# Performance work log

Measured on AMD Instinct MI355X. Metric: run time of the kernel, lower is better.

Reference implementation:

```python
import jax, jax.numpy as jnp
import numpy as np

B_, L_, D_MODEL = 2, 1024, 1024
D_STATE, EXPAND = 16, 2
D_INNER = EXPAND * D_MODEL            # 2048
DT_RANK = (D_MODEL + 15) // 16        # 64


def setup_inputs() -> dict:
    key = jax.random.key(0)
    ks = jax.random.split(key, 6)
    dt_min, dt_max, dt_floor = 1e-3, 0.1, 1e-4
    dt = jnp.exp(jax.random.uniform(ks[4], (D_INNER,)) * (np.log(dt_max) - np.log(dt_min)) + np.log(dt_min))
    dt = jnp.clip(dt, dt_floor)
    inv_dt = dt + jnp.log(-jnp.expm1(-dt))  # softplus^{-1}(dt), matches torch init
    A_log = jnp.log(jnp.broadcast_to(jnp.arange(1, D_STATE + 1, dtype=jnp.float32), (D_INNER, D_STATE)))
    s_in = 1.0 / np.sqrt(D_MODEL)
    s_inner = 1.0 / np.sqrt(D_INNER)
    return {
        "input_states": jax.random.normal(ks[0], (B_, L_, D_MODEL), jnp.float32),
        "in_proj_w": jax.random.normal(ks[1], (2 * D_INNER, D_MODEL), jnp.float32) * s_in,
        "x_proj_w": jax.random.normal(ks[2], (DT_RANK + 2 * D_STATE, D_INNER), jnp.float32) * s_inner,
        "dt_proj_w": jax.random.uniform(ks[3], (D_INNER, DT_RANK), jnp.float32, -1.0, 1.0) * (DT_RANK ** -0.5),
        "dt_proj_b": inv_dt.astype(jnp.float32),
        "A_log": A_log,
        "D": jnp.ones((D_INNER,), jnp.float32),
        "out_proj_w": jax.random.normal(ks[5], (D_MODEL, D_INNER), jnp.float32) * s_inner,
        "context_len": 2,
    }


def _linear_scan(a, u, axis):
    # h_t = a_t * h_{t-1} + u_t, h_{-1} = 0, parallel associative scan
    def comb(left, right):
        a_l, b_l = left
        a_r, b_r = right
        return (a_r * a_l, a_r * b_l + b_r)
    return jax.lax.associative_scan(comb, (a, u), axis=axis)[1]


def reference(input_states, in_proj_w, x_proj_w, dt_proj_w, dt_proj_b, A_log, D, out_proj_w, context_len):
    # context_len <= 2 => both tree refines use the chain tree; feature_out = 1.3 * chain_tree_scan
    assert context_len <= 2, "MST branch (context_len>2) not modeled"
    b, L, _ = input_states.shape
    proj = input_states @ in_proj_w.T                       # (b, L, 2*d_inner)
    hidden, gate = jnp.split(proj, 2, axis=-1)              # (b, L, d)
    hs = jnp.swapaxes(hidden, 1, 2)                         # (b, d, L)
    ssm = hidden @ x_proj_w.T                               # (b, L, dt_rank+2n)
    dt, Bm, Cm = jnp.split(ssm, [DT_RANK, DT_RANK + D_STATE], axis=-1)
    dt = jax.nn.softplus(dt @ dt_proj_w.T + dt_proj_b)      # (b, L, d)
    dt_bdl = jnp.swapaxes(dt, 1, 2)                         # (b, d, L)
    A = -jnp.exp(A_log)                                     # (d, n)
    discrete_A = jnp.exp(A[None, :, None, :] * dt_bdl[:, :, :, None])           # (b, d, L, n)
    deltaB_u = dt_bdl[:, :, :, None] * Bm[:, None, :, :] * hs[:, :, :, None]    # (b, d, L, n)
    # chain tree filter: out[t] = sum_s prod(path A) * u[s] = fwd_scan + bwd_scan - u
    fwd = _linear_scan(discrete_A, deltaB_u, axis=2)
    a_rev = jnp.roll(jnp.flip(discrete_A, axis=2), 1, axis=2)  # == `weight` in source
    bwd = jnp.flip(_linear_scan(a_rev, jnp.flip(deltaB_u, axis=2), axis=2), axis=2)
    feature_out = (fwd + bwd - deltaB_u) * 1.3               # feature_out1 + 0.3*feature_out2
    y = jnp.einsum("bdln,bln->bdl", feature_out, Cm)         # (b, d, L)
    scan_output = (y + hs * D[None, :, None]) * jax.nn.silu(jnp.swapaxes(gate, 1, 2))
    return jnp.swapaxes(scan_output, 1, 2) @ out_proj_w.T    # (b, L, d_model)
```

## Files before the change

kernel.cpp:

```cpp
#include <hip/hip_runtime.h>
#include <hip/hip_bf16.h>
#include <cstdint>
#include <cstddef>

typedef __hip_bfloat16 bf16;
typedef __attribute__((ext_vector_type(8))) short short8v;
typedef __attribute__((ext_vector_type(4))) float f32x4;

__global__ __launch_bounds__(256)
void cast_bf16(const float* __restrict__ in, ushort* __restrict__ out, int n4)
{
    const int i = blockIdx.x * 256 + threadIdx.x;
    if (i >= n4) return;
    const float4 v = ((const float4*)in)[i];
    ushort4 o;
    bf16 h;
    h = __float2bfloat16(v.x); o.x = *(ushort*)&h;
    h = __float2bfloat16(v.y); o.y = *(ushort*)&h;
    h = __float2bfloat16(v.z); o.z = *(ushort*)&h;
    h = __float2bfloat16(v.w); o.w = *(ushort*)&h;
    ((ushort4*)out)[i] = o;
}

__global__ __launch_bounds__(256)
void gemm_bf16_mfma(const bf16* __restrict__ A, int lda,
                    const bf16* __restrict__ W, int ldw,
                    float* __restrict__ C, int ldc, int K)
{
    __shared__ short Asl[128 * 32];
    __shared__ short Wsl[128 * 32];
    const int tid = threadIdx.x;
    const int lane = tid & 63, wave = tid >> 6;
    const int row0 = blockIdx.y * 128, col0 = blockIdx.x * 128;
    const int wr = wave >> 1, wc = wave & 1;
    const int lr = lane & 15, lq = lane >> 4;

    f32x4 acc[4][4] = {};

    for (int k0 = 0; k0 < K; k0 += 32) {
#pragma unroll
        for (int i = 0; i < 2; ++i) {
            const int o = ((i * 4 + wave) << 9) + lane * 8;
            const int r = o >> 5, kk = o & 31;
            __builtin_amdgcn_global_load_lds(
                (const __attribute__((address_space(1))) void*)(A + (size_t)(row0 + r) * lda + k0 + kk),
                (__attribute__((address_space(3))) void*)(Asl + (((i * 4 + wave) << 9))),
                16, 0, 0);
            __builtin_amdgcn_global_load_lds(
                (const __attribute__((address_space(1))) void*)(W + (size_t)(col0 + r) * ldw + k0 + kk),
                (__attribute__((address_space(3))) void*)(Wsl + (((i * 4 + wave) << 9))),
                16, 0, 0);
        }
        __syncthreads();

        short8v af[4], wf[4];
#pragma unroll
        for (int m = 0; m < 4; ++m)
            af[m] = *(const short8v*)&Asl[(wr * 64 + m * 16 + lr) * 32 + lq * 8];
#pragma unroll
        for (int n = 0; n < 4; ++n)
            wf[n] = *(const short8v*)&Wsl[(wc * 64 + n * 16 + lr) * 32 + lq * 8];
#pragma unroll
        for (int m = 0; m < 4; ++m)
#pragma unroll
            for (int n = 0; n < 4; ++n)
                acc[m][n] = __builtin_amdgcn_mfma_f32_16x16x32_bf16(af[m], wf[n], acc[m][n], 0, 0, 0);
        __syncthreads();
    }

#pragma unroll
    for (int m = 0; m < 4; ++m) {
        const int r = row0 + wr * 64 + m * 16 + lq * 4;
#pragma unroll
        for (int n = 0; n < 4; ++n) {
            const int c = col0 + wc * 64 + n * 16 + lr;
#pragma unroll
            for (int j = 0; j < 4; ++j)
                C[(size_t)(r + j) * ldc + c] = acc[m][n][j];
        }
    }
}

#define BM 64
#define BN 64
#define BK 16
#define BMP 68
#define BNP 68

__global__ __launch_bounds__(256)
void gemm_nt(const float* __restrict__ A, int lda,
             const float* __restrict__ W, int ldw,
             float* __restrict__ C, int ldc,
             int M, int N, int K,
             const float* __restrict__ bias, int mode)
{
    __shared__ float As[BK][BMP];
    __shared__ float Ws[BK][BNP];

    const int tid  = threadIdx.x;
    const int row0 = blockIdx.y * BM;
    const int col0 = blockIdx.x * BN;
    const int lr = tid >> 2;
    const int lk = (tid & 3) << 2;
    const int tx = tid & 15;
    const int ty = tid >> 4;

    float acc[4][4];
#pragma unroll
    for (int i = 0; i < 4; ++i)
#pragma unroll
        for (int j = 0; j < 4; ++j) acc[i][j] = 0.f;

    for (int k0 = 0; k0 < K; k0 += BK) {
        float4 av = make_float4(0.f, 0.f, 0.f, 0.f);
        float4 wv = make_float4(0.f, 0.f, 0.f, 0.f);
        const int ar = row0 + lr;
        if (ar < M) av = *(const float4*)(A + (size_t)ar * lda + k0 + lk);
        const int wr = col0 + lr;
        if (wr < N) wv = *(const float4*)(W + (size_t)wr * ldw + k0 + lk);

        As[lk + 0][lr] = av.x; As[lk + 1][lr] = av.y;
        As[lk + 2][lr] = av.z; As[lk + 3][lr] = av.w;
        Ws[lk + 0][lr] = wv.x; Ws[lk + 1][lr] = wv.y;
        Ws[lk + 2][lr] = wv.z; Ws[lk + 3][lr] = wv.w;
        __syncthreads();

#pragma unroll
        for (int kk = 0; kk < BK; ++kk) {
            float4 a = *(const float4*)&As[kk][ty * 4];
            float4 w = *(const float4*)&Ws[kk][tx * 4];
            float ai[4] = {a.x, a.y, a.z, a.w};
            float wj[4] = {w.x, w.y, w.z, w.w};
#pragma unroll
            for (int i = 0; i < 4; ++i)
#pragma unroll
                for (int j = 0; j < 4; ++j)
                    acc[i][j] = fmaf(ai[i], wj[j], acc[i][j]);
        }
        __syncthreads();
    }

#pragma unroll
    for (int i = 0; i < 4; ++i) {
        const int r = row0 + ty * 4 + i;
        if (r >= M) continue;
#pragma unroll
        for (int j = 0; j < 4; ++j) {
            const int c = col0 + tx * 4 + j;
            if (c >= N) continue;
            float v = acc[i][j];
            if (mode == 1) {
                v += bias[c];
                v = (v > 20.f) ? v : log1pf(__expf(v));
            }
            C[(size_t)r * ldc + c] = v;
        }
    }
}

__global__ __launch_bounds__(256)
void gemm_nt_splitk(const float* __restrict__ A, int lda,
                    const float* __restrict__ W, int ldw,
                    float* __restrict__ P,
                    int M, int N, int K, int ksplit)
{
    __shared__ float As[BK][BMP];
    __shared__ float Ws[BK][BNP];

    const int tid  = threadIdx.x;
    const int row0 = blockIdx.y * BM;
    const int col0 = blockIdx.x * BN;
    const int z    = blockIdx.z;
    const int k0s = z * ksplit, k0e = k0s + ksplit;
    const int lr = tid >> 2;
    const int lk = (tid & 3) << 2;
    const int tx = tid & 15;
    const int ty = tid >> 4;

    float acc[4][4];
#pragma unroll
    for (int i = 0; i < 4; ++i)
#pragma unroll
        for (int j = 0; j < 4; ++j) acc[i][j] = 0.f;

    for (int k0 = k0s; k0 < k0e; k0 += BK) {
        float4 av = make_float4(0.f, 0.f, 0.f, 0.f);
        float4 wv = make_float4(0.f, 0.f, 0.f, 0.f);
        const int ar = row0 + lr;
        if (ar < M) av = *(const float4*)(A + (size_t)ar * lda + k0 + lk);
        const int wr = col0 + lr;
        if (wr < N) wv = *(const float4*)(W + (size_t)wr * ldw + k0 + lk);

        As[lk + 0][lr] = av.x; As[lk + 1][lr] = av.y;
        As[lk + 2][lr] = av.z; As[lk + 3][lr] = av.w;
        Ws[lk + 0][lr] = wv.x; Ws[lk + 1][lr] = wv.y;
        Ws[lk + 2][lr] = wv.z; Ws[lk + 3][lr] = wv.w;
        __syncthreads();

#pragma unroll
        for (int kk = 0; kk < BK; ++kk) {
            float4 a = *(const float4*)&As[kk][ty * 4];
            float4 w = *(const float4*)&Ws[kk][tx * 4];
            float ai[4] = {a.x, a.y, a.z, a.w};
            float wj[4] = {w.x, w.y, w.z, w.w};
#pragma unroll
            for (int i = 0; i < 4; ++i)
#pragma unroll
                for (int j = 0; j < 4; ++j)
                    acc[i][j] = fmaf(ai[i], wj[j], acc[i][j]);
        }
        __syncthreads();
    }

    float* C = P + (size_t)z * M * N;
#pragma unroll
    for (int i = 0; i < 4; ++i) {
        const int r = row0 + ty * 4 + i;
        if (r >= M) continue;
#pragma unroll
        for (int j = 0; j < 4; ++j) {
            const int c = col0 + tx * 4 + j;
            if (c >= N) continue;
            C[(size_t)r * N + c] = acc[i][j];
        }
    }
}

__global__ __launch_bounds__(256)
void reduce_splitk(const float* __restrict__ P, float* __restrict__ out,
                   int total, int nsplit)
{
    const int i = blockIdx.x * 256 + threadIdx.x;
    if (i >= total) return;
    float s = 0.f;
    for (int z = 0; z < nsplit; ++z) s += P[i + (size_t)z * total];
    out[i] = s;
}

#define NC 32
#define CL 32
#define DI 2048
#define NST 16

__global__ __launch_bounds__(256)
void scan_chunk_local(const float* __restrict__ proj,
                      const float* __restrict__ ssm,
                      const float* __restrict__ dtb,
                      const float* __restrict__ A_log,
                      float* __restrict__ Pf, float* __restrict__ He,
                      float* __restrict__ Pb, float* __restrict__ Gs,
                      float* __restrict__ dtbound)
{
    const int g = blockIdx.x * 256 + threadIdx.x;
    const int d = g & (DI - 1);
    const int r = g >> 11;
    const int c = r & (NC - 1);
    const int b = r >> 5;
    const int t0 = c * CL;
    const size_t rowbase = (size_t)b * 1024;

    float Av[NST];
#pragma unroll
    for (int n = 0; n < NST; ++n) Av[n] = -__expf(A_log[d * NST + n]);

    float h[NST], pf[NST];
#pragma unroll
    for (int n = 0; n < NST; ++n) { h[n] = 0.f; pf[n] = 1.f; }
    for (int t = t0; t < t0 + CL; ++t) {
        const size_t row = rowbase + t;
        const float dtv = dtb[row * DI + d];
        const float hv  = proj[row * 4096 + d];
        const float dh  = dtv * hv;
#pragma unroll
        for (int n = 0; n < NST; ++n) {
            const float Bv = ssm[row * 96 + 64 + n];
            const float dA = __expf(Av[n] * dtv);
            h[n] = fmaf(dA, h[n], dh * Bv);
            pf[n] *= dA;
        }
    }
    const size_t ibase = ((size_t)((b * NC + c) * NST) << 11) + d;
#pragma unroll
    for (int n = 0; n < NST; ++n) {
        Pf[ibase + ((size_t)n << 11)] = pf[n];
        He[ibase + ((size_t)n << 11)] = h[n];
    }

    float dtn = INFINITY;
    const int t1 = t0 + CL;
    if (t1 < 1024) dtn = dtb[(rowbase + t1) * DI + d];
    dtbound[(size_t)(b * NC + c) * DI + d] = dtn;

    float gq[NST], pb[NST], dan[NST];
#pragma unroll
    for (int n = 0; n < NST; ++n) {
        gq[n] = 0.f; pb[n] = 1.f;
        dan[n] = __expf(Av[n] * dtn);
    }
    for (int t = t0 + CL - 1; t >= t0; --t) {
        const size_t row = rowbase + t;
        const float dtv = dtb[row * DI + d];
        const float hv  = proj[row * 4096 + d];
        const float dh  = dtv * hv;
#pragma unroll
        for (int n = 0; n < NST; ++n) {
            const float Bv = ssm[row * 96 + 64 + n];
            gq[n] = fmaf(dan[n], gq[n], dh * Bv);
            pb[n] *= dan[n];
            dan[n] = __expf(Av[n] * dtv);
        }
    }
#pragma unroll
    for (int n = 0; n < NST; ++n) {
        Pb[ibase + ((size_t)n << 11)] = pb[n];
        Gs[ibase + ((size_t)n << 11)] = gq[n];
    }
}

__global__ __launch_bounds__(256)
void scan_combine(const float* __restrict__ Pf, float* __restrict__ He,
                  const float* __restrict__ Pb, float* __restrict__ Gs)
{
    const int g = blockIdx.x * 256 + threadIdx.x;
    const int d = g & (DI - 1);
    const int r = g >> 11;
    const int n = r & (NST - 1);
    const int b = r >> 4;
    const size_t base = ((size_t)(b * NC * NST + n) << 11) + d;
    const size_t cstride = (size_t)NST << 11;

    float H = 0.f;
    for (int c = 0; c < NC; ++c) {
        const size_t i = base + (size_t)c * cstride;
        const float p = Pf[i], e = He[i];
        He[i] = H;
        H = fmaf(p, H, e);
    }
    float G = 0.f;
    for (int c = NC - 1; c >= 0; --c) {
        const size_t i = base + (size_t)c * cstride;
        const float p = Pb[i], s = Gs[i];
        Gs[i] = G;
        G = fmaf(p, G, s);
    }
}

__global__ __launch_bounds__(256)
void scan_apply(const float* __restrict__ proj,
                const float* __restrict__ ssm,
                const float* __restrict__ dtb,
                const float* __restrict__ A_log,
                const float* __restrict__ Dvec,
                const float* __restrict__ He,
                const float* __restrict__ Gs,
                const float* __restrict__ dtbound,
                ushort* __restrict__ sob)
{
    __shared__ float ybuf[256][CL + 1];
    const int tid = threadIdx.x;
    const int g = blockIdx.x * 256 + tid;
    const int d = g & (DI - 1);
    const int r = g >> 11;
    const int c = r & (NC - 1);
    const int b = r >> 5;
    const int t0 = c * CL;
    const size_t rowbase = (size_t)b * 1024;

    float Av[NST];
#pragma unroll
    for (int n = 0; n < NST; ++n) Av[n] = -__expf(A_log[d * NST + n]);
    const size_t ibase = ((size_t)((b * NC + c) * NST) << 11) + d;

    float h[NST];
#pragma unroll
    for (int n = 0; n < NST; ++n) h[n] = He[ibase + ((size_t)n << 11)];
    for (int t = t0; t < t0 + CL; ++t) {
        const size_t row = rowbase + t;
        const float dtv = dtb[row * DI + d];
        const float hv  = proj[row * 4096 + d];
        const float dh  = dtv * hv;
        float y = 0.f;
#pragma unroll
        for (int n = 0; n < NST; ++n) {
            const float Bv = ssm[row * 96 + 64 + n];
            const float Cv = ssm[row * 96 + 80 + n];
            const float dA = __expf(Av[n] * dtv);
            h[n] = fmaf(dA, h[n], dh * Bv);
            y = fmaf(h[n], Cv, y);
        }
        ybuf[tid][t - t0] = y;
    }

    float gq[NST], dan[NST];
#pragma unroll
    for (int n = 0; n < NST; ++n) gq[n] = Gs[ibase + ((size_t)n << 11)];
    {
        const float dtn = dtbound[(size_t)(b * NC + c) * DI + d];
#pragma unroll
        for (int n = 0; n < NST; ++n) dan[n] = __expf(Av[n] * dtn);
    }
    const float Dd = Dvec[d];
    for (int t = t0 + CL - 1; t >= t0; --t) {
        const size_t row = rowbase + t;
        const float dtv = dtb[row * DI + d];
        const float hv  = proj[row * 4096 + d];
        const float dh  = dtv * hv;
        float acc = 0.f;
#pragma unroll
        for (int n = 0; n < NST; ++n) {
            const float Bv = ssm[row * 96 + 64 + n];
            const float Cv = ssm[row * 96 + 80 + n];
            const float u  = dh * Bv;
            gq[n] = fmaf(dan[n], gq[n], u);
            dan[n] = __expf(Av[n] * dtv);
            acc = fmaf(gq[n] - u, Cv, acc);
        }
        const float y   = (ybuf[tid][t - t0] + acc) * 1.3f;
        const float gv  = proj[row * 4096 + DI + d];
        const float sil = gv / (1.f + __expf(-gv));
        const float val = (y + hv * Dd) * sil;
        bf16 hb = __float2bfloat16(val);
        sob[row * DI + d] = *(ushort*)&hb;
    }
}

extern "C" void kernel_launch(void* const* d_in, const int* in_sizes, int n_in,
                              void* d_out, int out_size, void* d_ws, size_t ws_size,
                              hipStream_t stream)
{
    const float* x     = (const float*)d_in[0];
    const float* Win   = (const float*)d_in[1];
    const float* Wx    = (const float*)d_in[2];
    const float* Wdt   = (const float*)d_in[3];
    const float* bdt   = (const float*)d_in[4];
    const float* A_log = (const float*)d_in[5];
    const float* Dv    = (const float*)d_in[6];
    const float* Wout  = (const float*)d_in[7];
    float* out = (float*)d_out;

    const int B = 2, L = 1024, DM = 1024;
    const int M = B * L;

    float* proj = (float*)d_ws;
    float* ssm  = proj + (size_t)M * 2 * DI;
    float* dtb  = ssm  + (size_t)M * 96;
    float* Pf   = dtb  + (size_t)M * DI;
    float* He   = Pf   + (size_t)B * NC * NST * DI;
    float* Pb   = He   + (size_t)B * NC * NST * DI;
    float* Gs   = Pb   + (size_t)B * NC * NST * DI;
    float* dtbd = Gs   + (size_t)B * NC * NST * DI;
    ushort* xb    = (ushort*)(dtbd + (size_t)B * NC * DI);
    ushort* Winb  = xb    + (size_t)M * DM;
    ushort* Woutb = Winb  + (size_t)(2 * DI) * DM;
    ushort* sob   = Woutb + (size_t)DM * DI;
    float* part = Pf;

    dim3 blk(256);

    cast_bf16<<<dim3((M * DM / 4) / 256), blk, 0, stream>>>(x, xb, M * DM / 4);
    cast_bf16<<<dim3((2 * DI * DM / 4) / 256), blk, 0, stream>>>(Win, Winb, 2 * DI * DM / 4);
    cast_bf16<<<dim3((DM * DI / 4) / 256), blk, 0, stream>>>(Wout, Woutb, DM * DI / 4);

    gemm_bf16_mfma<<<dim3((2 * DI) / 128, M / 128), blk, 0, stream>>>(
        (const bf16*)xb, DM, (const bf16*)Winb, DM, proj, 2 * DI, DM);

    gemm_nt_splitk<<<dim3(2, M / BM, 16), blk, 0, stream>>>(
        proj, 2 * DI, Wx, DI, part, M, 96, DI, DI / 16);
    reduce_splitk<<<dim3((M * 96 + 255) / 256), blk, 0, stream>>>(
        part, ssm, M * 96, 16);

    gemm_nt<<<dim3(DI / BN, M / BM), blk, 0, stream>>>(
        ssm, 96, Wdt, 64, dtb, DI, M, DI, 64, bdt, 1);

    scan_chunk_local<<<dim3((B * DI * NC) / 256), blk, 0, stream>>>(
        proj, ssm, dtb, A_log, Pf, He, Pb, Gs, dtbd);
    scan_combine<<<dim3((B * DI * NST) / 256), blk, 0, stream>>>(Pf, He, Pb, Gs);
    scan_apply<<<dim3((B * DI * NC) / 256), blk, 0, stream>>>(
        proj, ssm, dtb, A_log, Dv, He, Gs, dtbd, sob);

    gemm_bf16_mfma<<<dim3(DM / 128, M / 128), blk, 0, stream>>>(
        (const bf16*)sob, DI, (const bf16*)Woutb, DI, out, DM, DI);
}
```

Before: 315.0 us.

## Split scan state dimension across thread pairs and fuse backward chunk pass

Each (batch, chunk, channel) scan task is now handled by two adjacent threads, each owning 8 of the 16 state entries, with y and acc partial sums combined via lane shuffles. This doubles the thread count and halves per-thread registers and serial work to raise occupancy. The chunk-local kernel also drops its separate backward pass, computing the backward chunk sum and product algebraically inside the forward loop with a running prefix product. Adjacent lanes now read the same d, so dtb/proj loads are duplicated and less coalesced per thread, and only half the lanes write the output.

```diff
diff --git a/kernel.cpp b/kernel.cpp
--- a/kernel.cpp
+++ b/kernel.cpp
@@ -252,68 +252,64 @@
                       float* __restrict__ dtbound)
 {
     const int g = blockIdx.x * 256 + threadIdx.x;
-    const int d = g & (DI - 1);
-    const int r = g >> 11;
+    const int half = g & 1;
+    const int d = (g >> 1) & (DI - 1);
+    const int r = g >> 12;
     const int c = r & (NC - 1);
     const int b = r >> 5;
     const int t0 = c * CL;
+    const int n0 = half * 8;
     const size_t rowbase = (size_t)b * 1024;
 
-    float Av[NST];
-#pragma unroll
-    for (int n = 0; n < NST; ++n) Av[n] = -__expf(A_log[d * NST + n]);
-
-    float h[NST], pf[NST];
-#pragma unroll
-    for (int n = 0; n < NST; ++n) { h[n] = 0.f; pf[n] = 1.f; }
-    for (int t = t0; t < t0 + CL; ++t) {
+    float Av[8];
+#pragma unroll
+    for (int n = 0; n < 8; ++n) Av[n] = -__expf(A_log[d * NST + n0 + n]);
+
+    float h[8], pf[8], gs[8], pq[8];
+    {
+        const size_t row = rowbase + t0;
+        const float dtv = dtb[row * DI + d];
+        const float hv  = proj[row * 4096 + d];
+        const float dh  = dtv * hv;
+#pragma unroll
+        for (int n = 0; n < 8; ++n) {
+            const float Bv = ssm[row * 96 + 64 + n0 + n];
+            const float u  = dh * Bv;
+            pf[n] = __expf(Av[n] * dtv);
+            h[n] = u; gs[n] = u; pq[n] = 1.f;
+        }
+    }
+    for (int t = t0 + 1; t < t0 + CL; ++t) {
         const size_t row = rowbase + t;
         const float dtv = dtb[row * DI + d];
         const float hv  = proj[row * 4096 + d];
         const float dh  = dtv * hv;
 #pragma unroll
-        for (int n = 0; n < NST; ++n) {
-            const float Bv = ssm[row * 96 + 64 + n];
+        for (int n = 0; n < 8; ++n) {
+            const float Bv = ssm[row * 96 + 64 + n0 + n];
             const float dA = __expf(Av[n] * dtv);
-            h[n] = fmaf(dA, h[n], dh * Bv);
+            const float u  = dh * Bv;
+            h[n]  = fmaf(dA, h[n], u);
             pf[n] *= dA;
-        }
-    }
-    const size_t ibase = ((size_t)((b * NC + c) * NST) << 11) + d;
-#pragma unroll
-    for (int n = 0; n < NST; ++n) {
-        Pf[ibase + ((size_t)n << 11)] = pf[n];
-        He[ibase + ((size_t)n << 11)] = h[n];
+            pq[n] *= dA;
+            gs[n] = fmaf(pq[n], u, gs[n]);
+        }
     }
 
     float dtn = INFINITY;
     const int t1 = t0 + CL;
     if (t1 < 1024) dtn = dtb[(rowbase + t1) * DI + d];
-    dtbound[(size_t)(b * NC + c) * DI + d] = dtn;
-
-    float gq[NST], pb[NST], dan[NST];
-#pragma unroll
-    for (int n = 0; n < NST; ++n) {
-        gq[n] = 0.f; pb[n] = 1.f;
-        dan[n] = __expf(Av[n] * dtn);
-    }
-    for (int t = t0 + CL - 1; t >= t0; --t) {
-        const size_t row = rowbase + t;
-        const float dtv = dtb[row * DI + d];
-        const float hv  = proj[row * 4096 + d];
-        const float dh  = dtv * hv;
-#pragma unroll
-        for (int n = 0; n < NST; ++n) {
-            const float Bv = ssm[row * 96 + 64 + n];
-            gq[n] = fmaf(dan[n], gq[n], dh * Bv);
-            pb[n] *= dan[n];
-            dan[n] = __expf(Av[n] * dtv);
-        }
-    }
-#pragma unroll
-    for (int n = 0; n < NST; ++n) {
-        Pb[ibase + ((size_t)n << 11)] = pb[n];
-        Gs[ibase + ((size_t)n << 11)] = gq[n];
+    if (half == 0) dtbound[(size_t)(b * NC + c) * DI + d] = dtn;
+
+    const size_t ibase = ((size_t)((b * NC + c) * NST) << 11) + d;
+#pragma unroll
+    for (int n = 0; n < 8; ++n) {
+        const float dAb = __expf(Av[n] * dtn);
+        const size_t o = ibase + ((size_t)(n0 + n) << 11);
+        Pf[o] = pf[n];
+        He[o] = h[n];
+        Pb[o] = pq[n] * dAb;
+        Gs[o] = gs[n];
     }
 }
 
@@ -359,68 +355,73 @@
     __shared__ float ybuf[256][CL + 1];
     const int tid = threadIdx.x;
     const int g = blockIdx.x * 256 + tid;
-    const int d = g & (DI - 1);
-    const int r = g >> 11;
+    const int half = g & 1;
+    const int d = (g >> 1) & (DI - 1);
+    const int r = g >> 12;
     const int c = r & (NC - 1);
     const int b = r >> 5;
     const int t0 = c * CL;
+    const int n0 = half * 8;
     const size_t rowbase = (size_t)b * 1024;
 
-    float Av[NST];
-#pragma unroll
-    for (int n = 0; n < NST; ++n) Av[n] = -__expf(A_log[d * NST + n]);
+    float Av[8];
+#pragma unroll
+    for (int n = 0; n < 8; ++n) Av[n] = -__expf(A_log[d * NST + n0 + n]);
     const size_t ibase = ((size_t)((b * NC + c) * NST) << 11) + d;
 
-    float h[NST];
-#pragma unroll
-    for (int n = 0; n < NST; ++n) h[n] = He[ibase + ((size_t)n << 11)];
-    for (int t = t0; t < t0 + CL; ++t) {
-        const size_t row = rowbase + t;
+    float h[8];
+#pragma unroll
+    for (int n = 0; n < 8; ++n) h[n] = He[ibase + ((size_t)(n0 + n) << 11)];
+    for (int i = 0; i < CL; ++i) {
+        const size_t row = rowbase + t0 + i;
         const float dtv = dtb[row * DI + d];
         const float hv  = proj[row * 4096 + d];
         const float dh  = dtv * hv;
         float y = 0.f;
 #pragma unroll
-        for (int n = 0; n < NST; ++n) {
-            const float Bv = ssm[row * 96 + 64 + n];
-            const float Cv = ssm[row * 96 + 80 + n];
+        for (int n = 0; n < 8; ++n) {
+            const float Bv = ssm[row * 96 + 64 + n0 + n];
+            const float Cv = ssm[row * 96 + 80 + n0 + n];
             const float dA = __expf(Av[n] * dtv);
             h[n] = fmaf(dA, h[n], dh * Bv);
             y = fmaf(h[n], Cv, y);
         }
-        ybuf[tid][t - t0] = y;
-    }
-
-    float gq[NST], dan[NST];
-#pragma unroll
-    for (int n = 0; n < NST; ++n) gq[n] = Gs[ibase + ((size_t)n << 11)];
+        ybuf[tid][i] = y + __shfl_xor(y, 1);
+    }
+
+    float gq[8], dan[8];
+#pragma unroll
+    for (int n = 0; n < 8; ++n) gq[n] = Gs[ibase + ((size_t)(n0 + n) << 11)];
     {
         const float dtn = dtbound[(size_t)(b * NC + c) * DI + d];
 #pragma unroll
-        for (int n = 0; n < NST; ++n) dan[n] = __expf(Av[n] * dtn);
+        for (int n = 0; n < 8; ++n) dan[n] = __expf(Av[n] * dtn);
     }
     const float Dd = Dvec[d];
-    for (int t = t0 + CL - 1; t >= t0; --t) {
-        const size_t row = rowbase + t;
+    for (int i = CL - 1; i >= 0; --i) {
+        const size_t row = rowbase + t0 + i;
         const float dtv = dtb[row * DI + d];
         const float hv  = proj[row * 4096 + d];
         const float dh  = dtv * hv;
         float acc = 0.f;
 #pragma unroll
-        for (int n = 0; n < NST; ++n) {
-            const float Bv = ssm[row * 96 + 64 + n];
-            const float Cv = ssm[row * 96 + 80 + n];
+        for (int n = 0; n < 8; ++n) {
+            const float Bv = ssm[row * 96 + 64 + n0 + n];
+            const float Cv = ssm[row * 96 + 80 + n0 + n];
             const float u  = dh * Bv;
             gq[n] = fmaf(dan[n], gq[n], u);
             dan[n] = __expf(Av[n] * dtv);
             acc = fmaf(gq[n] - u, Cv, acc);
         }
-        const float y   = (ybuf[tid][t - t0] + acc) * 1.3f;
-        const float gv  = proj[row * 4096 + DI + d];
-        const float sil = gv / (1.f + __expf(-gv));
-        const float val = (y + hv * Dd) * sil;
-        bf16 hb = __float2bfloat16(val);
-        sob[row * DI + d] = *(ushort*)&hb;
+        acc += __shfl_xor(acc, 1);
+        if (half == 0) {
+            const float y   = (ybuf[tid][i] + acc) * 1.3f;
+            const float gv  = proj[row * 4096 + DI + d];
+            const float sil = gv / (1.f + __expf(-gv));
+            const float val = (y + hv * Dd) * sil;
+            bf16 hb = __float2bfloat16(val);
+            sob[row * DI + d] = *(ushort*)&hb;
+        }
     }
 }
 
@@ -472,10 +473,10 @@
     gemm_nt<<<dim3(DI / BN, M / BM), blk, 0, stream>>>(
         ssm, 96, Wdt, 64, dtb, DI, M, DI, 64, bdt, 1);
 
-    scan_chunk_local<<<dim3((B * DI * NC) / 256), blk, 0, stream>>>(
+    scan_chunk_local<<<dim3((B * DI * NC * 2) / 256), blk, 0, stream>>>(
         proj, ssm, dtb, A_log, Pf, He, Pb, Gs, dtbd);
     scan_combine<<<dim3((B * DI * NST) / 256), blk, 0, stream>>>(Pf, He, Pb, Gs);
-    scan_apply<<<dim3((B * DI * NC) / 256), blk, 0, stream>>>(
+    scan_apply<<<dim3((B * DI * NC * 2) / 256), blk, 0, stream>>>(
         proj, ssm, dtb, A_log, Dv, He, Gs, dtbd, sob);
 
     gemm_bf16_mfma<<<dim3(DM / 128, M / 128), blk, 0, stream>>>(
```

Result: no change. 308.9 us (-1.9%).
